# Performance work log

Hardware: AMD Instinct MI355X
Metric: run time of the kernel (lower is better)

The kernel has to match this reference:

```python
import jax, jax.numpy as jnp
import numpy as np

S, B, D, H, DFF = 1024, 8, 1024, 16, 4096
DH = D // H
EPS = 1e-5


def setup_inputs() -> dict:
    key = jax.random.key(0)
    ks = jax.random.split(key, 20)
    w = lambda k, shape: (jax.random.normal(k, shape, jnp.float32) * 0.02)
    return {
        "x": jax.random.normal(ks[0], (S, B, D), jnp.float32),
        "key_padding_mask": jax.random.randint(ks[1], (B, S), 0, 5) == 0,
        "attn_bias": jax.random.uniform(ks[2], (B, 1, S), jnp.float32),
        "Wq": w(ks[3], (D, D)), "bq": jnp.zeros((D,), jnp.float32),
        "Wk": w(ks[4], (D, D)), "bk": jnp.zeros((D,), jnp.float32),
        "Wv": w(ks[5], (D, D)), "bv": jnp.zeros((D,), jnp.float32),
        "Wo": w(ks[6], (D, D)), "bo": jnp.zeros((D,), jnp.float32),
        "W1": w(ks[7], (D, DFF)), "b1": jnp.zeros((DFF,), jnp.float32),
        "W2": w(ks[8], (DFF, D)), "b2": jnp.zeros((D,), jnp.float32),
        "g1": jnp.ones((D,), jnp.float32), "be1": jnp.zeros((D,), jnp.float32),
        "g2": jnp.ones((D,), jnp.float32), "be2": jnp.zeros((D,), jnp.float32),
        "alpha": jnp.asarray(0.1, jnp.float32),
    }


def _ln(x, g, b):
    m = jnp.mean(x, axis=-1, keepdims=True)
    v = jnp.mean(jnp.square(x - m), axis=-1, keepdims=True)
    return (x - m) * jax.lax.rsqrt(v + EPS) * g + b


def reference(x, key_padding_mask, attn_bias, Wq, bq, Wk, bk, Wv, bv, Wo, bo,
              W1, b1, W2, b2, g1, be1, g2, be2, alpha):
    # x: (S, B, D) seq-first; pre-norm attention block
    x2 = _ln(x, g1, be1).transpose(1, 0, 2)  # (B, S, D)
    def heads(W, bias):
        return (x2 @ W + bias).reshape(B, S, H, DH).transpose(0, 2, 1, 3)  # (B,H,S,DH)
    Q, K, V = heads(Wq, bq), heads(Wk, bk), heads(Wv, bv)
    scores = jnp.einsum('bhqd,bhkd->bhqk', Q, K) * (DH ** -0.5)  # (B,H,S,S)
    # attn_bias (B,1,S) -> (B,1,1,S): additive key-side TF-IDF bias
    scores = scores + attn_bias[:, :, None, :] * alpha
    scores = jnp.where(key_padding_mask[:, None, None, :], -jnp.inf, scores)
    attn = jax.nn.softmax(scores, axis=-1)
    out = jnp.einsum('bhqk,bhkd->bhqd', attn, V)  # (B,H,S,DH)
    out = out.transpose(0, 2, 1, 3).reshape(B, S, D)
    out = (out @ Wo + bo).transpose(1, 0, 2)  # back to (S,B,D)
    x = x + out
    # pre-norm FFN block
    h = _ln(x, g2, be2)
    h = jax.nn.relu(h @ W1 + b1) @ W2 + b2
    return x + h
```

## Files before the change

kernel.cpp:

```cpp
#include <hip/hip_runtime.h>
#include <stdint.h>

#define S_LEN 1024
#define BATCH 8
#define DMODEL 1024
#define NHEAD 16
#define DHEAD 64
#define DFF_N 4096
#define EPS 1e-5f

typedef __attribute__((ext_vector_type(8))) short bf16x8;
typedef __attribute__((ext_vector_type(4))) float f32x4;

__device__ __forceinline__ unsigned short f2bf(float f) {
  union { float f; unsigned u; } x; x.f = f;
  unsigned r = x.u + 0x7FFFu + ((x.u >> 16) & 1u);
  return (unsigned short)(r >> 16);
}

__device__ __forceinline__ void gld_lds16(const void* g, void* l) {
  __builtin_amdgcn_global_load_lds(
      (const __attribute__((address_space(1))) void*)g,
      (__attribute__((address_space(3))) void*)l, 16, 0, 0);
}

#define BARRIER asm volatile("s_barrier" ::: "memory")

__global__ __launch_bounds__(256) void transpose_cvt(
    const float* __restrict__ src, unsigned short* __restrict__ dst, int K, int N) {
  __shared__ float tile[32][33];
  int n0 = blockIdx.x * 32, k0 = blockIdx.y * 32;
  int tx = threadIdx.x & 31, ty = threadIdx.x >> 5;
#pragma unroll
  for (int p = 0; p < 4; ++p)
    tile[ty + p * 8][tx] = src[(long)(k0 + ty + p * 8) * N + n0 + tx];
  __syncthreads();
#pragma unroll
  for (int p = 0; p < 4; ++p)
    dst[(long)(n0 + ty + p * 8) * K + k0 + tx] = f2bf(tile[tx][ty + p * 8]);
}

__global__ __launch_bounds__(256) void biasm_kernel(
    const float* __restrict__ bias, const int* __restrict__ kpm,
    const float* __restrict__ alpha_p, float* __restrict__ biasm) {
  int i = blockIdx.x * 256 + threadIdx.x;
  float a = alpha_p[0];
  biasm[i] = kpm[i] ? -1e30f : bias[i] * a;
}

__global__ __launch_bounds__(256) void ln_kernel(
    const float* __restrict__ in, const float* __restrict__ g,
    const float* __restrict__ be, unsigned short* __restrict__ out, int permute) {
  int rr = blockIdx.x;
  long in_off;
  if (permute) { int b = rr >> 10, s = rr & 1023; in_off = ((long)s * BATCH + b) * DMODEL; }
  else in_off = (long)rr * DMODEL;
  int t = threadIdx.x;
  float4 v = *(const float4*)(in + in_off + t * 4);
  float sum = v.x + v.y + v.z + v.w;
#pragma unroll
  for (int m = 1; m < 64; m <<= 1) sum += __shfl_xor(sum, m);
  __shared__ float red[4];
  __shared__ float red2[4];
  int wave = t >> 6, lane = t & 63;
  if (lane == 0) red[wave] = sum;
  __syncthreads();
  sum = red[0] + red[1] + red[2] + red[3];
  float mean = sum * (1.0f / DMODEL);
  float dx = v.x - mean, dy = v.y - mean, dz = v.z - mean, dw = v.w - mean;
  float vs = dx * dx + dy * dy + dz * dz + dw * dw;
#pragma unroll
  for (int m = 1; m < 64; m <<= 1) vs += __shfl_xor(vs, m);
  if (lane == 0) red2[wave] = vs;
  __syncthreads();
  vs = red2[0] + red2[1] + red2[2] + red2[3];
  float rstd = rsqrtf(vs * (1.0f / DMODEL) + EPS);
  float4 gv = *(const float4*)(g + t * 4);
  float4 bv = *(const float4*)(be + t * 4);
  ushort4 pk;
  pk.x = f2bf(dx * rstd * gv.x + bv.x);
  pk.y = f2bf(dy * rstd * gv.y + bv.y);
  pk.z = f2bf(dz * rstd * gv.z + bv.z);
  pk.w = f2bf(dw * rstd * gv.w + bv.w);
  *(ushort4*)(out + (long)rr * DMODEL + t * 4) = pk;
}

#define MODE_QKV 0
#define MODE_OPROJ 1
#define MODE_FFN1 2
#define MODE_FFN2 3

#define QUADW(MH, NH) do { \
  _Pragma("unroll") for (int i_ = 0; i_ < 4; ++i_) \
  _Pragma("unroll") for (int j_ = 0; j_ < 2; ++j_) \
  _Pragma("unroll") for (int k_ = 0; k_ < 2; ++k_) \
    acc[(MH) * 4 + i_][(NH) * 2 + j_] = __builtin_amdgcn_mfma_f32_16x16x32_bf16( \
        af[i_][k_], bfr[NH][j_][k_], acc[(MH) * 4 + i_][(NH) * 2 + j_], 0, 0, 0); \
} while (0)

#define QUADN(MH) do { \
  _Pragma("unroll") for (int i_ = 0; i_ < 2; ++i_) \
  _Pragma("unroll") for (int n_ = 0; n_ < 2; ++n_) \
  _Pragma("unroll") for (int j_ = 0; j_ < 2; ++j_) \
  _Pragma("unroll") for (int k_ = 0; k_ < 2; ++k_) \
    acc[(MH) * 2 + i_][n_ * 2 + j_] = __builtin_amdgcn_mfma_f32_16x16x32_bf16( \
        af[i_][k_], bfr[n_][j_][k_], acc[(MH) * 2 + i_][n_ * 2 + j_], 0, 0, 0); \
} while (0)

template <int MODE, bool WIDE>
__global__ __launch_bounds__(512, 2) void gemm_ph(
    const unsigned short* __restrict__ A, const unsigned short* __restrict__ Bt,
    int N, int K,
    const float* __restrict__ bias0, const float* __restrict__ bias1,
    const float* __restrict__ bias2,
    unsigned short* out_q, unsigned short* out_k, unsigned short* out_vt,
    const float* __restrict__ resid, float* out_f32, unsigned short* out_bf16) {
  constexpr int BNv = WIDE ? 256 : 128;
  constexpr int NM = WIDE ? 4 : 2;
  constexpr int BSLOT = WIDE ? 16384 : 8192;
  __shared__ unsigned short AS[32768];
  __shared__ unsigned short BS[WIDE ? 32768 : 16384];
  char* ASb = (char*)AS;
  char* BSb = (char*)BS;

  int nbx = gridDim.x;
  int nwg = nbx * gridDim.y;
  int orig = blockIdx.y * nbx + blockIdx.x;
  int swz = (orig & 7) * (nwg >> 3) + (orig >> 3);
  int bx = swz % nbx, by = swz / nbx;
  int m0 = by * 256, n0 = bx * BNv;
  int tid = threadIdx.x, wave = tid >> 6, lane = tid & 63;
  int qr = lane & 15, g = lane >> 4, xh = qr & 7;
  int wr = WIDE ? (wave >> 2) : (wave >> 1);
  int wc = WIDE ? (wave & 3) : (wave & 1);
  int srow = wave * 8 + (lane >> 3);
  int sgo = ((lane & 7) ^ (lane >> 3)) * 8;
  const long rK64 = (long)K * 64;
  const unsigned short* AbS = A + (long)m0 * K + (long)srow * K + sgo;
  const unsigned short* BbS = Bt + (long)n0 * K + (long)srow * K + sgo;
  int c0 = (g ^ xh) * 16;
  int c1 = ((4 + g) ^ xh) * 16;
  int roA = (WIDE ? wr * 64 : wr * 32) + qr;
  int roB = wc * 32 + qr;

  f32x4 acc[2 * NM][4];
#pragma unroll
  for (int i = 0; i < 2 * NM; ++i)
#pragma unroll
    for (int j = 0; j < 4; ++j) acc[i][j] = (f32x4){0.f, 0.f, 0.f, 0.f};
  bf16x8 af[NM][2];
  bf16x8 bfr[2][2][2];

  auto stA = [&](int kt, int slot, int L) {
    gld_lds16(AbS + slot * 2 * rK64 + L * rK64 + kt * 64,
              ASb + ((kt & 1) * 2 + slot) * 16384 + L * 8192 + wave * 1024);
  };
  auto stB = [&](int kt, int slot, int L) {
    if constexpr (WIDE)
      gld_lds16(BbS + slot * 2 * rK64 + L * rK64 + kt * 64,
                BSb + ((kt & 1) * 2 + slot) * 16384 + L * 8192 + wave * 1024);
    else
      gld_lds16(BbS + slot * rK64 + kt * 64,
                BSb + ((kt & 1) * 2 + slot) * 8192 + wave * 1024);
  };
  auto ldAh = [&](int buf, int mh) {
    const char* base = ASb + (buf * 2 + mh) * 16384 + roA * 128;
#pragma unroll
    for (int i = 0; i < NM; ++i) {
      af[i][0] = *(const bf16x8*)(base + i * 2048 + c0);
      af[i][1] = *(const bf16x8*)(base + i * 2048 + c1);
    }
  };
  auto ldBh = [&](bf16x8 (&bq)[2][2], int buf, int nh) {
    const char* base = BSb + (buf * 2 + nh) * BSLOT + roB * 128;
#pragma unroll
    for (int j = 0; j < 2; ++j) {
      bq[j][0] = *(const bf16x8*)(base + j * 2048 + c0);
      bq[j][1] = *(const bf16x8*)(base + j * 2048 + c1);
    }
  };

  const int NT = K / 64;
  if constexpr (WIDE) {
    stA(0, 0, 0); stA(0, 0, 1); stA(0, 1, 0); stA(0, 1, 1);
    stB(0, 0, 0); stB(0, 0, 1); stB(0, 1, 0); stB(0, 1, 1);
    stA(1, 0, 0); stA(1, 0, 1); stB(1, 0, 0); stB(1, 0, 1); stB(1, 1, 0); stB(1, 1, 1);
    asm volatile("s_waitcnt vmcnt(6)" ::: "memory");
  } else {
    stA(0, 0, 0); stA(0, 0, 1); stA(0, 1, 0); stA(0, 1, 1);
    stB(0, 0, 0); stB(0, 1, 0);
    stA(1, 0, 0); stA(1, 0, 1); stB(1, 0, 0); stB(1, 1, 0);
    asm volatile("s_waitcnt vmcnt(4)" ::: "memory");
  }
  __builtin_amdgcn_sched_barrier(0);
  BARRIER;

  for (int kt = 0; kt < NT; ++kt) {
    int buf = kt & 1;
    if constexpr (WIDE) {
      ldAh(buf, 0);
      ldBh(bfr[0], buf, 0);
      if (kt + 1 < NT) { stA(kt + 1, 1, 0); stA(kt + 1, 1, 1); }
      BARRIER; __builtin_amdgcn_sched_barrier(0);
      __builtin_amdgcn_s_setprio(1); QUADW(0, 0); __builtin_amdgcn_s_setprio(0);
      BARRIER;
      ldBh(bfr[1], buf, 1);
      if (kt + 2 < NT) { stA(kt + 2, 0, 0); stA(kt + 2, 0, 1); }
      BARRIER; __builtin_amdgcn_sched_barrier(0);
      __builtin_amdgcn_s_setprio(1); QUADW(0, 1); __builtin_amdgcn_s_setprio(0);
      BARRIER;
      ldAh(buf, 1);
      if (kt + 2 < NT) { stB(kt + 2, 0, 0); stB(kt + 2, 0, 1); }
      BARRIER; __builtin_amdgcn_sched_barrier(0);
      __builtin_amdgcn_s_setprio(1); QUADW(1, 1); __builtin_amdgcn_s_setprio(0);
      BARRIER;
      if (kt + 2 < NT) { stB(kt + 2, 1, 0); stB(kt + 2, 1, 1); }
      BARRIER; __builtin_amdgcn_sched_barrier(0);
      __builtin_amdgcn_s_setprio(1); QUADW(1, 0); __builtin_amdgcn_s_setprio(0);
      if (kt + 2 < NT) asm volatile("s_waitcnt vmcnt(6)" ::: "memory");
      else asm volatile("s_waitcnt vmcnt(0)" ::: "memory");
      __builtin_amdgcn_sched_barrier(0);
      BARRIER;
    } else {
      ldAh(buf, 0);
      ldBh(bfr[0], buf, 0);
      ldBh(bfr[1], buf, 1);
      if (kt + 1 < NT) { stA(kt + 1, 1, 0); stA(kt + 1, 1, 1); }
      BARRIER; __builtin_amdgcn_sched_barrier(0);
      __builtin_amdgcn_s_setprio(1); QUADN(0); __builtin_amdgcn_s_setprio(0);
      BARRIER;
      ldAh(buf, 1);
      if (kt + 2 < NT) { stA(kt + 2, 0, 0); stA(kt + 2, 0, 1); stB(kt + 2, 0, 0); stB(kt + 2, 1, 0); }
      BARRIER; __builtin_amdgcn_sched_barrier(0);
      __builtin_amdgcn_s_setprio(1); QUADN(1); __builtin_amdgcn_s_setprio(0);
      if (kt + 2 < NT) asm volatile("s_waitcnt vmcnt(4)" ::: "memory");
      else asm volatile("s_waitcnt vmcnt(0)" ::: "memory");
      __builtin_amdgcn_sched_barrier(0);
      BARRIER;
    }
  }

#pragma unroll
  for (int I = 0; I < 2 * NM; ++I) {
#pragma unroll
    for (int J = 0; J < 4; ++J) {
      int mrow, ncol;
      if constexpr (WIDE) {
        mrow = m0 + (I >> 2) * 128 + wr * 64 + (I & 3) * 16 + g * 4;
        ncol = n0 + (J >> 1) * 128 + wc * 32 + (J & 1) * 16 + qr;
      } else {
        mrow = m0 + (I >> 1) * 128 + wr * 32 + (I & 1) * 16 + g * 4;
        ncol = n0 + (J >> 1) * 64 + wc * 32 + (J & 1) * 16 + qr;
      }
      if constexpr (MODE == MODE_QKV) {
        int sel = ncol >> 10, nn = ncol & 1023;
        int h = nn >> 6, dh = nn & 63;
        const float* bptr = (sel == 0) ? bias0 : ((sel == 1) ? bias1 : bias2);
        float bias = bptr[nn];
        if (sel < 2) {
          unsigned short* dst = (sel == 0) ? out_q : out_k;
#pragma unroll
          for (int r = 0; r < 4; ++r) {
            int m = mrow + r; int bb = m >> 10, s = m & 1023;
            dst[(((long)(bb * NHEAD + h)) * S_LEN + s) * DHEAD + dh] = f2bf(acc[I][J][r] + bias);
          }
        } else {
          int m = mrow; int bb = m >> 10, s = m & 1023;
          ushort4 pk;
          pk.x = f2bf(acc[I][J][0] + bias);
          pk.y = f2bf(acc[I][J][1] + bias);
          pk.z = f2bf(acc[I][J][2] + bias);
          pk.w = f2bf(acc[I][J][3] + bias);
          *(ushort4*)&out_vt[(((long)(bb * NHEAD + h)) * DHEAD + dh) * S_LEN + s] = pk;
        }
      } else if constexpr (MODE == MODE_OPROJ) {
        float bias = bias0[ncol];
#pragma unroll
        for (int r = 0; r < 4; ++r) {
          int m = mrow + r; int bb = m >> 10, s = m & 1023;
          long oi = ((long)s * BATCH + bb) * DMODEL + ncol;
          out_f32[oi] = resid[oi] + acc[I][J][r] + bias;
        }
      } else if constexpr (MODE == MODE_FFN1) {
        float bias = bias0[ncol];
#pragma unroll
        for (int r = 0; r < 4; ++r) {
          long m = mrow + r;
          float v = acc[I][J][r] + bias;
          out_bf16[m * (long)N + ncol] = f2bf(v > 0.f ? v : 0.f);
        }
      } else {
        float bias = bias0[ncol];
#pragma unroll
        for (int r = 0; r < 4; ++r) {
          long m = mrow + r;
          long oi = m * (long)N + ncol;
          out_f32[oi] = resid[oi] + acc[I][J][r] + bias;
        }
      }
    }
  }
}

__global__ __launch_bounds__(512, 4) void attn_kernel(
    const unsigned short* __restrict__ qbuf, const unsigned short* __restrict__ kbuf,
    const unsigned short* __restrict__ vtbuf, const float* __restrict__ biasm,
    unsigned short* __restrict__ out) {
  int wave = threadIdx.x >> 6, lane = threadIdx.x & 63;
  int h = blockIdx.y, b = blockIdx.z;
  int q0 = blockIdx.x * 256 + wave * 32;
  long bh = (long)(b * NHEAD + h);
  const unsigned short* Q = qbuf + bh * S_LEN * DHEAD;
  const unsigned short* Kp = kbuf + bh * S_LEN * DHEAD;
  const unsigned short* Vt = vtbuf + bh * DHEAD * S_LEN;
  const float* bm = biasm + (long)b * S_LEN;

  __shared__ unsigned short Ktile[2][64 * 64];
  __shared__ unsigned short Vtile[2][64 * 64];
  __shared__ uint2 Pbuf[8][256];
  __shared__ float AL[8][2][16];
  __shared__ float LI[8][2][16];
  uint2* Pw = Pbuf[wave];

  int qr = lane & 15, g = lane >> 4;

  int srow = wave * 8 + (lane >> 3);
  int scol = (lane & 7) ^ (srow & 7);
  const unsigned short* Ksrc = Kp + (long)srow * DHEAD + scol * 8;
  const unsigned short* Vsrc = Vt + (long)srow * S_LEN + scol * 8;

  bf16x8 qf[2][2];
#pragma unroll
  for (int f = 0; f < 2; ++f)
#pragma unroll
    for (int dhh = 0; dhh < 2; ++dhh)
      qf[f][dhh] = *(const bf16x8*)&Q[(long)(q0 + f * 16 + qr) * DHEAD + dhh * 32 + g * 8];

  f32x4 oacc[2][4];
#pragma unroll
  for (int f = 0; f < 2; ++f)
#pragma unroll
    for (int dt = 0; dt < 4; ++dt) oacc[f][dt] = (f32x4){0.f, 0.f, 0.f, 0.f};
  float m_[2] = {-1e30f, -1e30f}, l_[2] = {0.f, 0.f};

  auto stage = [&](int k0s, int buf) {
    gld_lds16(Ksrc + (long)k0s * DHEAD, (char*)&Ktile[buf][0] + wave * 1024);
    gld_lds16(Vsrc + k0s, (char*)&Vtile[buf][0] + wave * 1024);
  };

  stage(0, 0);
  int cur = 0;
  const int NT = S_LEN / 64;
  for (int t = 0; t < NT; ++t) {
    __syncthreads();
    if (t + 1 < NT) stage((t + 1) * 64, cur ^ 1);

    const char* Kt_l = (const char*)&Ktile[cur][0];
    f32x4 sacc[2][4];
#pragma unroll
    for (int f = 0; f < 2; ++f)
#pragma unroll
      for (int n = 0; n < 4; ++n) sacc[f][n] = (f32x4){0.f, 0.f, 0.f, 0.f};
#pragma unroll
    for (int n = 0; n < 4; ++n)
#pragma unroll
      for (int dhh = 0; dhh < 2; ++dhh) {
        bf16x8 kf = *(const bf16x8*)(Kt_l + (n * 16 + qr) * 128 + (((dhh * 4 + g) ^ (qr & 7)) * 16));
        sacc[0][n] = __builtin_amdgcn_mfma_f32_16x16x32_bf16(kf, qf[0][dhh], sacc[0][n], 0, 0, 0);
        sacc[1][n] = __builtin_amdgcn_mfma_f32_16x16x32_bf16(kf, qf[1][dhh], sacc[1][n], 0, 0, 0);
      }
    float4 bv[4];
#pragma unroll
    for (int n = 0; n < 4; ++n) bv[n] = *(const float4*)&bm[t * 64 + n * 16 + g * 4];

    bf16x8 paf[2][2];
#pragma unroll
    for (int f = 0; f < 2; ++f) {
      float s[16];
#pragma unroll
      for (int n = 0; n < 4; ++n) {
        const float* bvp = (const float*)&bv[n];
#pragma unroll
        for (int r = 0; r < 4; ++r) s[n * 4 + r] = fmaf(sacc[f][n][r], 0.125f, bvp[r]);
      }
      float mx = s[0];
#pragma unroll
      for (int i = 1; i < 16; ++i) mx = fmaxf(mx, s[i]);
      mx = fmaxf(mx, __shfl_xor(mx, 16));
      mx = fmaxf(mx, __shfl_xor(mx, 32));
      float mnew = fmaxf(m_[f], mx);
      float al = __expf(m_[f] - mnew);
      m_[f] = mnew;
      float ps = 0.f;
#pragma unroll
      for (int i = 0; i < 16; ++i) { s[i] = __expf(s[i] - mnew); ps += s[i]; }
      ps += __shfl_xor(ps, 16);
      ps += __shfl_xor(ps, 32);
      l_[f] = l_[f] * al + ps;
      if (lane < 16) AL[wave][f][lane] = al;
#pragma unroll
      for (int n = 0; n < 4; ++n) {
        unsigned w0, w1;
        asm("v_cvt_pk_bf16_f32 %0, %1, %2" : "=v"(w0) : "v"(s[n * 4 + 0]), "v"(s[n * 4 + 1]));
        asm("v_cvt_pk_bf16_f32 %0, %1, %2" : "=v"(w1) : "v"(s[n * 4 + 2]), "v"(s[n * 4 + 3]));
        Pw[qr * 16 + ((n * 4 + g) ^ qr)] = (uint2){w0, w1};
      }
#pragma unroll
      for (int kb = 0; kb < 2; ++kb) {
        union { uint2 u[2]; bf16x8 v; } p;
        p.u[0] = Pw[qr * 16 + ((kb * 8 + g * 2 + 0) ^ qr)];
        p.u[1] = Pw[qr * 16 + ((kb * 8 + g * 2 + 1) ^ qr)];
        paf[f][kb] = p.v;
      }
    }
#pragma unroll
    for (int f = 0; f < 2; ++f) {
      float4 alv = *(const float4*)&AL[wave][f][g * 4];
      const float* ap = (const float*)&alv;
#pragma unroll
      for (int dt = 0; dt < 4; ++dt)
#pragma unroll
        for (int r = 0; r < 4; ++r) oacc[f][dt][r] *= ap[r];
    }
    const char* Vt_l = (const char*)&Vtile[cur][0];
#pragma unroll
    for (int dt = 0; dt < 4; ++dt)
#pragma unroll
      for (int kb = 0; kb < 2; ++kb) {
        bf16x8 vf = *(const bf16x8*)(Vt_l + (dt * 16 + qr) * 128 + (((kb * 4 + g) ^ (qr & 7)) * 16));
        oacc[0][dt] = __builtin_amdgcn_mfma_f32_16x16x32_bf16(paf[0][kb], vf, oacc[0][dt], 0, 0, 0);
        oacc[1][dt] = __builtin_amdgcn_mfma_f32_16x16x32_bf16(paf[1][kb], vf, oacc[1][dt], 0, 0, 0);
      }
    cur ^= 1;
  }

#pragma unroll
  for (int f = 0; f < 2; ++f)
    if (lane < 16) LI[wave][f][lane] = 1.0f / l_[f];
#pragma unroll
  for (int f = 0; f < 2; ++f) {
    float4 lv = *(const float4*)&LI[wave][f][g * 4];
    const float* lp = (const float*)&lv;
#pragma unroll
    for (int dt = 0; dt < 4; ++dt)
#pragma unroll
      for (int r = 0; r < 4; ++r) {
        int q = q0 + f * 16 + g * 4 + r;
        int dh = dt * 16 + qr;
        out[((long)(b * S_LEN + q)) * DMODEL + h * DHEAD + dh] = f2bf(oacc[f][dt][r] * lp[r]);
      }
  }
}

extern "C" void kernel_launch(void* const* d_in, const int* in_sizes, int n_in,
                              void* d_out, int out_size, void* d_ws, size_t ws_size,
                              hipStream_t stream) {
  const float* x  = (const float*)d_in[0];
  const int* kpm  = (const int*)d_in[1];
  const float* attn_bias = (const float*)d_in[2];
  const float* Wq = (const float*)d_in[3];  const float* bq = (const float*)d_in[4];
  const float* Wk = (const float*)d_in[5];  const float* bk = (const float*)d_in[6];
  const float* Wv = (const float*)d_in[7];  const float* bv = (const float*)d_in[8];
  const float* Wo = (const float*)d_in[9];  const float* bo = (const float*)d_in[10];
  const float* W1 = (const float*)d_in[11]; const float* b1 = (const float*)d_in[12];
  const float* W2 = (const float*)d_in[13]; const float* b2 = (const float*)d_in[14];
  const float* g1 = (const float*)d_in[15]; const float* be1 = (const float*)d_in[16];
  const float* g2 = (const float*)d_in[17]; const float* be2 = (const float*)d_in[18];
  const float* alpha = (const float*)d_in[19];
  float* out = (float*)d_out;

  char* ws = (char*)d_ws;
  size_t off = 0;
  auto alloc = [&](size_t bytes) { void* p = ws + off; off += (bytes + 255) & ~(size_t)255; return p; };
  unsigned short* WqkvT = (unsigned short*)alloc(3072ull * 1024 * 2);
  unsigned short* WoT   = (unsigned short*)alloc(1024ull * 1024 * 2);
  unsigned short* W1T   = (unsigned short*)alloc(4096ull * 1024 * 2);
  unsigned short* W2T   = (unsigned short*)alloc(1024ull * 4096 * 2);
  float* biasm          = (float*)alloc(8192ull * 4);
  float* y1             = (float*)alloc(8192ull * 1024 * 4);
  char* region = (char*)alloc(5ull * 16 * 1024 * 1024);
  unsigned short* x2     = (unsigned short*)(region);
  unsigned short* qb     = (unsigned short*)(region + 16ull * 1024 * 1024);
  unsigned short* kb     = (unsigned short*)(region + 32ull * 1024 * 1024);
  unsigned short* vtb    = (unsigned short*)(region + 48ull * 1024 * 1024);
  unsigned short* attn_o = (unsigned short*)(region + 64ull * 1024 * 1024);
  unsigned short* h2     = (unsigned short*)(region);
  unsigned short* ffn1   = (unsigned short*)(region + 16ull * 1024 * 1024);

  transpose_cvt<<<dim3(32, 32), 256, 0, stream>>>(Wq, WqkvT, 1024, 1024);
  transpose_cvt<<<dim3(32, 32), 256, 0, stream>>>(Wk, WqkvT + 1024ull * 1024, 1024, 1024);
  transpose_cvt<<<dim3(32, 32), 256, 0, stream>>>(Wv, WqkvT + 2048ull * 1024, 1024, 1024);
  transpose_cvt<<<dim3(32, 32), 256, 0, stream>>>(Wo, WoT, 1024, 1024);
  transpose_cvt<<<dim3(128, 32), 256, 0, stream>>>(W1, W1T, 1024, 4096);
  transpose_cvt<<<dim3(32, 128), 256, 0, stream>>>(W2, W2T, 4096, 1024);

  biasm_kernel<<<32, 256, 0, stream>>>(attn_bias, kpm, alpha, biasm);
  ln_kernel<<<8192, 256, 0, stream>>>(x, g1, be1, x2, 1);

  gemm_ph<MODE_QKV, false><<<dim3(3072 / 128, 32), 512, 0, stream>>>(
      x2, WqkvT, 3072, 1024, bq, bk, bv, qb, kb, vtb, nullptr, nullptr, nullptr);

  attn_kernel<<<dim3(S_LEN / 256, NHEAD, BATCH), 512, 0, stream>>>(
      qb, kb, vtb, biasm, attn_o);

  gemm_ph<MODE_OPROJ, false><<<dim3(1024 / 128, 32), 512, 0, stream>>>(
      attn_o, WoT, 1024, 1024, bo, nullptr, nullptr,
      nullptr, nullptr, nullptr, x, y1, nullptr);

  ln_kernel<<<8192, 256, 0, stream>>>(y1, g2, be2, h2, 0);

  gemm_ph<MODE_FFN1, true><<<dim3(4096 / 256, 32), 512, 0, stream>>>(
      h2, W1T, 4096, 1024, b1, nullptr, nullptr,
      nullptr, nullptr, nullptr, nullptr, nullptr, ffn1);

  gemm_ph<MODE_FFN2, false><<<dim3(1024 / 128, 32), 512, 0, stream>>>(
      ffn1, W2T, 1024, 4096, b2, nullptr, nullptr,
      nullptr, nullptr, nullptr, y1, out, nullptr);
}
```

Measured before the change: 499.7 us.

## Fuse prep kernels, widen QKV tiles, split-K FFN2, tree-reduce softmax

Folds the six weight transpose/convert launches and the bias-mask launch into a single prep kernel to cut launch overhead. Switches the QKV GEMM to the wide 256-column tile and runs FFN2 as a two-way split-K GEMM whose partials are stored as bf16 and summed with residual and bias by a new reduce kernel. In attention, the per-row max and sum become tree reductions, and each fragment gets its own P scratch buffer, which doubles that shared-memory allocation. Rounding the split-K partials to bf16 adds precision loss, and the extra reduce pass adds memory traffic.

```diff
diff --git a/kernel.cpp b/kernel.cpp
--- a/kernel.cpp
+++ b/kernel.cpp
@@ -17,6 +17,9 @@
   unsigned r = x.u + 0x7FFFu + ((x.u >> 16) & 1u);
   return (unsigned short)(r >> 16);
 }
+__device__ __forceinline__ float bf2f(unsigned short u) {
+  union { unsigned u; float f; } x; x.u = ((unsigned)u) << 16; return x.f;
+}
 
 __device__ __forceinline__ void gld_lds16(const void* g, void* l) {
   __builtin_amdgcn_global_load_lds(
@@ -26,26 +29,40 @@
 
 #define BARRIER asm volatile("s_barrier" ::: "memory")
 
-__global__ __launch_bounds__(256) void transpose_cvt(
-    const float* __restrict__ src, unsigned short* __restrict__ dst, int K, int N) {
-  __shared__ float tile[32][33];
-  int n0 = blockIdx.x * 32, k0 = blockIdx.y * 32;
-  int tx = threadIdx.x & 31, ty = threadIdx.x >> 5;
-#pragma unroll
-  for (int p = 0; p < 4; ++p)
-    tile[ty + p * 8][tx] = src[(long)(k0 + ty + p * 8) * N + n0 + tx];
-  __syncthreads();
-#pragma unroll
-  for (int p = 0; p < 4; ++p)
-    dst[(long)(n0 + ty + p * 8) * K + k0 + tx] = f2bf(tile[tx][ty + p * 8]);
-}
-
-__global__ __launch_bounds__(256) void biasm_kernel(
+__global__ __launch_bounds__(256) void prep_kernel(
+    const float* __restrict__ Wq, const float* __restrict__ Wk,
+    const float* __restrict__ Wv, const float* __restrict__ Wo,
+    const float* __restrict__ W1, const float* __restrict__ W2,
+    unsigned short* __restrict__ WqkvT, unsigned short* __restrict__ WoT,
+    unsigned short* __restrict__ W1T, unsigned short* __restrict__ W2T,
     const float* __restrict__ bias, const int* __restrict__ kpm,
     const float* __restrict__ alpha_p, float* __restrict__ biasm) {
-  int i = blockIdx.x * 256 + threadIdx.x;
-  float a = alpha_p[0];
-  biasm[i] = kpm[i] ? -1e30f : bias[i] * a;
+  int bid = blockIdx.x;
+  if (bid < 32) {
+    int i = bid * 256 + threadIdx.x;
+    float a = alpha_p[0];
+    biasm[i] = kpm[i] ? -1e30f : bias[i] * a;
+    return;
+  }
+  bid -= 32;
+  const float* src; unsigned short* dst; int K, N, tile;
+  if (bid < 1024)      { src = Wq; dst = WqkvT;                 K = 1024; N = 1024; tile = bid; }
+  else if (bid < 2048) { src = Wk; dst = WqkvT + 1024 * 1024;   K = 1024; N = 1024; tile = bid - 1024; }
+  else if (bid < 3072) { src = Wv; dst = WqkvT + 2048 * 1024;   K = 1024; N = 1024; tile = bid - 2048; }
+  else if (bid < 4096) { src = Wo; dst = WoT;                   K = 1024; N = 1024; tile = bid - 3072; }
+  else if (bid < 8192) { src = W1; dst = W1T;                   K = 1024; N = 4096; tile = bid - 4096; }
+  else                 { src = W2; dst = W2T;                   K = 4096; N = 1024; tile = bid - 8192; }
+  int nx = N >> 5;
+  int n0 = (tile % nx) * 32, k0 = (tile / nx) * 32;
+  __shared__ float tilebuf[32][33];
+  int tx = threadIdx.x & 31, ty = threadIdx.x >> 5;
+#pragma unroll
+  for (int p = 0; p < 4; ++p)
+    tilebuf[ty + p * 8][tx] = src[(long)(k0 + ty + p * 8) * N + n0 + tx];
+  __syncthreads();
+#pragma unroll
+  for (int p = 0; p < 4; ++p)
+    dst[(long)(n0 + ty + p * 8) * K + k0 + tx] = f2bf(tilebuf[tx][ty + p * 8]);
 }
 
 __global__ __launch_bounds__(256) void ln_kernel(
@@ -85,10 +102,29 @@
   *(ushort4*)(out + (long)rr * DMODEL + t * 4) = pk;
 }
 
+__global__ __launch_bounds__(256) void ffn2_reduce(
+    const unsigned short* __restrict__ p0, const unsigned short* __restrict__ p1,
+    const float* __restrict__ resid, const float* __restrict__ b2,
+    float* __restrict__ out) {
+  long i = ((long)blockIdx.x * 256 + threadIdx.x) * 4;
+  ushort4 a = *(const ushort4*)(p0 + i);
+  ushort4 b = *(const ushort4*)(p1 + i);
+  float4 r = *(const float4*)(resid + i);
+  int nc = (int)(i & 1023);
+  float4 bb = *(const float4*)(b2 + nc);
+  float4 o;
+  o.x = bf2f(a.x) + bf2f(b.x) + r.x + bb.x;
+  o.y = bf2f(a.y) + bf2f(b.y) + r.y + bb.y;
+  o.z = bf2f(a.z) + bf2f(b.z) + r.z + bb.z;
+  o.w = bf2f(a.w) + bf2f(b.w) + r.w + bb.w;
+  *(float4*)(out + i) = o;
+}
+
 #define MODE_QKV 0
 #define MODE_OPROJ 1
 #define MODE_FFN1 2
 #define MODE_FFN2 3
+#define MODE_PART 4
 
 #define QUADW(MH, NH) do { \
   _Pragma("unroll") for (int i_ = 0; i_ < 4; ++i_) \
@@ -110,7 +146,7 @@
 template <int MODE, bool WIDE>
 __global__ __launch_bounds__(512, 2) void gemm_ph(
     const unsigned short* __restrict__ A, const unsigned short* __restrict__ Bt,
-    int N, int K,
+    int N, int K, int NT,
     const float* __restrict__ bias0, const float* __restrict__ bias1,
     const float* __restrict__ bias2,
     unsigned short* out_q, unsigned short* out_k, unsigned short* out_vt,
@@ -129,6 +165,7 @@
   int swz = (orig & 7) * (nwg >> 3) + (orig >> 3);
   int bx = swz % nbx, by = swz / nbx;
   int m0 = by * 256, n0 = bx * BNv;
+  int kbase = blockIdx.z * NT * 64;
   int tid = threadIdx.x, wave = tid >> 6, lane = tid & 63;
   int qr = lane & 15, g = lane >> 4, xh = qr & 7;
   int wr = WIDE ? (wave >> 2) : (wave >> 1);
@@ -136,8 +173,8 @@
   int srow = wave * 8 + (lane >> 3);
   int sgo = ((lane & 7) ^ (lane >> 3)) * 8;
   const long rK64 = (long)K * 64;
-  const unsigned short* AbS = A + (long)m0 * K + (long)srow * K + sgo;
-  const unsigned short* BbS = Bt + (long)n0 * K + (long)srow * K + sgo;
+  const unsigned short* AbS = A + (long)m0 * K + (long)srow * K + sgo + kbase;
+  const unsigned short* BbS = Bt + (long)n0 * K + (long)srow * K + sgo + kbase;
   int c0 = (g ^ xh) * 16;
   int c1 = ((4 + g) ^ xh) * 16;
   int roA = (WIDE ? wr * 64 : wr * 32) + qr;
@@ -180,7 +217,6 @@
     }
   };
 
-  const int NT = K / 64;
   if constexpr (WIDE) {
     stA(0, 0, 0); stA(0, 0, 1); stA(0, 1, 0); stA(0, 1, 1);
     stB(0, 0, 0); stB(0, 0, 1); stB(0, 1, 0); stB(0, 1, 1);
@@ -289,6 +325,13 @@
           float v = acc[I][J][r] + bias;
           out_bf16[m * (long)N + ncol] = f2bf(v > 0.f ? v : 0.f);
         }
+      } else if constexpr (MODE == MODE_PART) {
+        unsigned short* pb = out_bf16 + (long)blockIdx.z * 8192 * N;
+#pragma unroll
+        for (int r = 0; r < 4; ++r) {
+          long m = mrow + r;
+          pb[m * (long)N + ncol] = f2bf(acc[I][J][r]);
+        }
       } else {
         float bias = bias0[ncol];
 #pragma unroll
@@ -317,7 +360,7 @@
 
   __shared__ unsigned short Ktile[2][64 * 64];
   __shared__ unsigned short Vtile[2][64 * 64];
-  __shared__ uint2 Pbuf[8][256];
+  __shared__ uint2 Pbuf[8][512];
   __shared__ float AL[8][2][16];
   __shared__ float LI[8][2][16];
   uint2* Pw = Pbuf[wave];
@@ -383,17 +426,25 @@
 #pragma unroll
         for (int r = 0; r < 4; ++r) s[n * 4 + r] = fmaf(sacc[f][n][r], 0.125f, bvp[r]);
       }
-      float mx = s[0];
-#pragma unroll
-      for (int i = 1; i < 16; ++i) mx = fmaxf(mx, s[i]);
+      float t8[8], t4[4];
+#pragma unroll
+      for (int i = 0; i < 8; ++i) t8[i] = fmaxf(s[i], s[i + 8]);
+#pragma unroll
+      for (int i = 0; i < 4; ++i) t4[i] = fmaxf(t8[i], t8[i + 4]);
+      float mx = fmaxf(fmaxf(t4[0], t4[1]), fmaxf(t4[2], t4[3]));
       mx = fmaxf(mx, __shfl_xor(mx, 16));
       mx = fmaxf(mx, __shfl_xor(mx, 32));
       float mnew = fmaxf(m_[f], mx);
       float al = __expf(m_[f] - mnew);
       m_[f] = mnew;
-      float ps = 0.f;
-#pragma unroll
-      for (int i = 0; i < 16; ++i) { s[i] = __expf(s[i] - mnew); ps += s[i]; }
+#pragma unroll
+      for (int i = 0; i < 16; ++i) s[i] = __expf(s[i] - mnew);
+      float u8[8], u4[4];
+#pragma unroll
+      for (int i = 0; i < 8; ++i) u8[i] = s[i] + s[i + 8];
+#pragma unroll
+      for (int i = 0; i < 4; ++i) u4[i] = u8[i] + u8[i + 4];
+      float ps = (u4[0] + u4[1]) + (u4[2] + u4[3]);
       ps += __shfl_xor(ps, 16);
       ps += __shfl_xor(ps, 32);
       l_[f] = l_[f] * al + ps;
@@ -403,13 +454,13 @@
         unsigned w0, w1;
         asm("v_cvt_pk_bf16_f32 %0, %1, %2" : "=v"(w0) : "v"(s[n * 4 + 0]), "v"(s[n * 4 + 1]));
         asm("v_cvt_pk_bf16_f32 %0, %1, %2" : "=v"(w1) : "v"(s[n * 4 + 2]), "v"(s[n * 4 + 3]));
-        Pw[qr * 16 + ((n * 4 + g) ^ qr)] = (uint2){w0, w1};
+        Pw[f * 256 + qr * 16 + ((n * 4 + g) ^ qr)] = (uint2){w0, w1};
       }
 #pragma unroll
       for (int kb = 0; kb < 2; ++kb) {
         union { uint2 u[2]; bf16x8 v; } p;
-        p.u[0] = Pw[qr * 16 + ((kb * 8 + g * 2 + 0) ^ qr)];
-        p.u[1] = Pw[qr * 16 + ((kb * 8 + g * 2 + 1) ^ qr)];
+        p.u[0] = Pw[f * 256 + qr * 16 + ((kb * 8 + g * 2 + 0) ^ qr)];
+        p.u[1] = Pw[f * 256 + qr * 16 + ((kb * 8 + g * 2 + 1) ^ qr)];
         paf[f][kb] = p.v;
       }
     }
@@ -486,34 +537,33 @@
   unsigned short* attn_o = (unsigned short*)(region + 64ull * 1024 * 1024);
   unsigned short* h2     = (unsigned short*)(region);
   unsigned short* ffn1   = (unsigned short*)(region + 16ull * 1024 * 1024);
-
-  transpose_cvt<<<dim3(32, 32), 256, 0, stream>>>(Wq, WqkvT, 1024, 1024);
-  transpose_cvt<<<dim3(32, 32), 256, 0, stream>>>(Wk, WqkvT + 1024ull * 1024, 1024, 1024);
-  transpose_cvt<<<dim3(32, 32), 256, 0, stream>>>(Wv, WqkvT + 2048ull * 1024, 1024, 1024);
-  transpose_cvt<<<dim3(32, 32), 256, 0, stream>>>(Wo, WoT, 1024, 1024);
-  transpose_cvt<<<dim3(128, 32), 256, 0, stream>>>(W1, W1T, 1024, 4096);
-  transpose_cvt<<<dim3(32, 128), 256, 0, stream>>>(W2, W2T, 4096, 1024);
-
-  biasm_kernel<<<32, 256, 0, stream>>>(attn_bias, kpm, alpha, biasm);
+  unsigned short* parts  = (unsigned short*)alloc(2ull * 8192 * 1024 * 2);
+
+  prep_kernel<<<12320, 256, 0, stream>>>(Wq, Wk, Wv, Wo, W1, W2,
+                                         WqkvT, WoT, W1T, W2T,
+                                         attn_bias, kpm, alpha, biasm);
+
   ln_kernel<<<8192, 256, 0, stream>>>(x, g1, be1, x2, 1);
 
-  gemm_ph<MODE_QKV, false><<<dim3(3072 / 128, 32), 512, 0, stream>>>(
-      x2, WqkvT, 3072, 1024, bq, bk, bv, qb, kb, vtb, nullptr, nullptr, nullptr);
+  gemm_ph<MODE_QKV, true><<<dim3(3072 / 256, 32), 512, 0, stream>>>(
+      x2, WqkvT, 3072, 1024, 16, bq, bk, bv, qb, kb, vtb, nullptr, nullptr, nullptr);
 
   attn_kernel<<<dim3(S_LEN / 256, NHEAD, BATCH), 512, 0, stream>>>(
       qb, kb, vtb, biasm, attn_o);
 
   gemm_ph<MODE_OPROJ, false><<<dim3(1024 / 128, 32), 512, 0, stream>>>(
-      attn_o, WoT, 1024, 1024, bo, nullptr, nullptr,
+      attn_o, WoT, 1024, 1024, 16, bo, nullptr, nullptr,
       nullptr, nullptr, nullptr, x, y1, nullptr);
 
   ln_kernel<<<8192, 256, 0, stream>>>(y1, g2, be2, h2, 0);
 
   gemm_ph<MODE_FFN1, true><<<dim3(4096 / 256, 32), 512, 0, stream>>>(
-      h2, W1T, 4096, 1024, b1, nullptr, nullptr,
+      h2, W1T, 4096, 1024, 16, b1, nullptr, nullptr,
       nullptr, nullptr, nullptr, nullptr, nullptr, ffn1);
 
-  gemm_ph<MODE_FFN2, false><<<dim3(1024 / 128, 32), 512, 0, stream>>>(
-      ffn1, W2T, 1024, 4096, b2, nullptr, nullptr,
-      nullptr, nullptr, nullptr, y1, out, nullptr);
-}
+  gemm_ph<MODE_PART, true><<<dim3(1024 / 256, 32, 2), 512, 0, stream>>>(
+      ffn1, W2T, 1024, 4096, 32, nullptr, nullptr, nullptr,
+      nullptr, nullptr, nullptr, nullptr, nullptr, parts);
+
+  ffn2_reduce<<<8192, 256, 0, stream>>>(parts, parts + 8192ull * 1024, y1, b2, out);
+}
```

Result: faster. 488.5 us (-2.2%).
